# Kernel tuning notes

Measured on AMD Instinct MI355X. Metric: run time of the kernel, lower is better.

The kernel has to match this reference:

```python
import jax, jax.numpy as jnp
import numpy as np

N_NODES = 100000
N_EDGES = 600000
D_IN = 128
HID = 128
N_LAYERS = 3


def gcn_conv(x, W, b, src, dst, num_nodes):
    """PyG-style GCNConv: D^{-1/2}(A+I)D^{-1/2} X W + b (self-loops added)."""
    h = x @ W  # [N, H]
    # in-degree including self-loop
    deg = jnp.zeros((num_nodes,), dtype=x.dtype).at[dst].add(1.0) + 1.0
    dinv = jax.lax.rsqrt(deg)
    norm = dinv[src] * dinv[dst]  # [E]
    msg = h[src] * norm[:, None]  # [E, H] gather + scale
    out = jax.ops.segment_sum(msg, dst, num_segments=num_nodes)  # scatter-add
    out = out + h * (1.0 / deg)[:, None]  # self-loop term (norm = 1/deg)
    return out + b


def setup_inputs() -> dict:
    key = jax.random.key(0)
    ks = jax.random.split(key, 16)
    x = jax.random.normal(ks[0], (N_NODES, D_IN), dtype=jnp.float32)
    edge_index = jax.random.randint(ks[1], (2, N_EDGES), 0, N_NODES, dtype=jnp.int64)
    timestamp = jax.random.uniform(ks[2], (1,), dtype=jnp.float32)
    # GCN layer weights (glorot-ish scale) and biases
    def glorot(k, fan_in, fan_out):
        s = jnp.sqrt(6.0 / (fan_in + fan_out))
        return jax.random.uniform(k, (fan_in, fan_out), minval=-s, maxval=s, dtype=jnp.float32)
    W_gcn = [glorot(ks[3], D_IN, HID), glorot(ks[4], HID, HID), glorot(ks[5], HID, HID)]
    b_gcn = [jnp.zeros((HID,), jnp.float32) for _ in range(N_LAYERS)]
    # temporal gate MLP: Linear(1,H) -> tanh -> Linear(H,H) -> sigmoid
    Wg1 = glorot(ks[6], 1, HID)
    bg1 = jnp.zeros((HID,), jnp.float32)
    Wg2 = glorot(ks[7], HID, HID)
    bg2 = jnp.zeros((HID,), jnp.float32)
    return {
        "x": x, "edge_index": edge_index, "timestamp": timestamp,
        "W0": W_gcn[0], "b0": b_gcn[0],
        "W1": W_gcn[1], "b1": b_gcn[1],
        "W2": W_gcn[2], "b2": b_gcn[2],
        "Wg1": Wg1, "bg1": bg1, "Wg2": Wg2, "bg2": bg2,
    }


def reference(x, edge_index, timestamp, W0, b0, W1, b1, W2, b2, Wg1, bg1, Wg2, bg2):
    src, dst = edge_index[0], edge_index[1]
    num_nodes = x.shape[0]
    # temporal gate: [1,1] -> [1,H], broadcast over nodes
    t = timestamp.reshape(1, 1)
    gate = jax.nn.sigmoid(jnp.tanh(t @ Wg1 + bg1) @ Wg2 + bg2)  # [1, H]
    for (W, b) in ((W0, b0), (W1, b1), (W2, b2)):
        x = gcn_conv(x, W, b, src, dst, num_nodes)
        x = jax.nn.relu(x)
        x = x * gate  # broadcast gate over nodes
        # dropout: identity in eval mode
    return x
```

## Files before the change

kernel.cpp:

```cpp
#include <hip/hip_runtime.h>
#include <hip/hip_bf16.h>
#include <hip/hip_fp16.h>
#include <math.h>


#define D 128

typedef __attribute__((ext_vector_type(8))) short short8;
typedef __attribute__((ext_vector_type(8))) _Float16 half8;
typedef __attribute__((ext_vector_type(4))) float floatx4;

#define RBITS 8
#define RSZ 256
#define SCAP 4096
#define RCAP 4096

__device__ __forceinline__ unsigned bf16_rne(float x) {
    unsigned u = __float_as_uint(x);
    return (u + 0x7FFFu + ((u >> 16) & 1u)) >> 16;
}

__device__ __forceinline__ void gload_lds16(const void* g, void* l) {
    __builtin_amdgcn_global_load_lds(
        (const __attribute__((address_space(1))) unsigned int*)g,
        (__attribute__((address_space(3))) unsigned int*)l, 16, 0, 0);
}

__device__ __forceinline__ float h2f(unsigned short u) {
    return __half2float(__ushort_as_half(u));
}

__device__ __forceinline__ int cap4(int c) { return (c + 3) & ~3; }

__global__ __launch_bounds__(256) void prep_kernel(
    const float* __restrict__ W0, const float* __restrict__ W1,
    const float* __restrict__ W2, short8* __restrict__ Wf_hi,
    short8* __restrict__ Wf_lo,
    const float* __restrict__ t, const float* __restrict__ Wg1,
    const float* __restrict__ bg1, const float* __restrict__ Wg2,
    const float* __restrict__ bg2, float* __restrict__ gate,
    int* __restrict__ cursor2, int B)
{
    int b = blockIdx.x;
    if (b < 24) {
        int f = b * 256 + threadIdx.x;
        int layer = f >> 11;
        int fi = f & 2047;
        int lane = fi & 63;
        int tt = fi >> 6;
        int kc = tt >> 3, n = tt & 7;
        const float* W = (layer == 0) ? W0 : (layer == 1) ? W1 : W2;
        int krow = kc * 32 + (lane >> 4) * 8;
        int col = n * 16 + (lane & 15);
        short8 hv, lv;
        if (layer == 0) {
            #pragma unroll
            for (int j = 0; j < 8; j++) {
                float x = W[(size_t)(krow + j) * D + col];
                unsigned hb = bf16_rne(x);
                float hf = __uint_as_float(hb << 16);
                unsigned lb = bf16_rne(x - hf);
                hv[j] = (short)hb;
                lv[j] = (short)lb;
            }
        } else {
            #pragma unroll
            for (int j = 0; j < 8; j++) {
                float x = W[(size_t)(krow + j) * D + col];
                __half hh = __float2half(x);
                float hf = __half2float(hh);
                __half ll = __float2half(x - hf);
                hv[j] = (short)__half_as_ushort(hh);
                lv[j] = (short)__half_as_ushort(ll);
            }
        }
        Wf_hi[f] = hv;
        Wf_lo[f] = lv;
        return;
    }
    for (int i = threadIdx.x; i < B; i += 256) cursor2[i] = i * SCAP;
    __shared__ float u[D];
    int j = threadIdx.x;
    if (j < D) {
        float tv = t[0];
        u[j] = tanhf(tv * Wg1[j] + bg1[j]);
    }
    __syncthreads();
    if (j < D) {
        float s = bg2[j];
        #pragma unroll 8
        for (int k = 0; k < D; k++) s += u[k] * Wg2[k * D + j];
        gate[j] = 1.0f / (1.0f + expf(-s));
    }
}

#define P1E 16
__global__ __launch_bounds__(256) void binpass_kernel(
    const int* __restrict__ w, int* __restrict__ cursor2,
    int2* __restrict__ stag, int E, int B)
{
    __shared__ int cnt[512];
    __shared__ int base[512];
    __shared__ int flag;
    int tid = threadIdx.x;
    if (tid == 0) {
        int z = 0;
        for (int k = 0; k < 64; k++) z |= w[2 * k + 1];
        flag = (z == 0) ? 1 : 0;
    }
    for (int i = tid; i < B; i += 256) cnt[i] = 0;
    __syncthreads();
    int i64 = flag;
    int e0 = blockIdx.x * (P1E * 256) + tid;
    int s[P1E], d[P1E], lp[P1E];
    #pragma unroll
    for (int k = 0; k < P1E; k++) {
        int e = e0 + k * 256;
        if (e < E) {
            s[k] = i64 ? w[2 * e] : w[e];
            d[k] = i64 ? w[2 * (E + e)] : w[E + e];
            lp[k] = atomicAdd(&cnt[d[k] >> RBITS], 1);
        }
    }
    __syncthreads();
    for (int i = tid; i < B; i += 256)
        base[i] = cnt[i] ? atomicAdd(&cursor2[i], cnt[i]) : 0;
    __syncthreads();
    #pragma unroll
    for (int k = 0; k < P1E; k++) {
        int e = e0 + k * 256;
        if (e < E) {
            int bin = d[k] >> RBITS;
            int idx = base[bin] + lp[k];
            if (idx < (bin + 1) * SCAP)
                stag[idx] = make_int2(s[k], d[k]);
        }
    }
}

__global__ __launch_bounds__(256) void place1_kernel(
    const int2* __restrict__ stag, const int* __restrict__ cursor2,
    int* __restrict__ obeg, int* __restrict__ oend,
    float* __restrict__ dinv, int N)
{
    __shared__ int cnt[RSZ];
    __shared__ int wsum[4], wpre[4];
    int b = blockIdx.x, tid = threadIdx.x;
    int d0 = b * RSZ;
    int nd = (d0 + RSZ < N) ? RSZ : N - d0;
    cnt[tid] = 0;
    __syncthreads();
    int ecount = cursor2[b] - b * SCAP;
    if (ecount > SCAP) ecount = SCAP;
    const int2* sp = stag + (size_t)b * SCAP;
    for (int i = tid; i < ecount; i += 256)
        atomicAdd(&cnt[sp[i].y - d0], 1);
    __syncthreads();
    int c = (tid < nd) ? cnt[tid] : 0;
    int cap = cap4(c);
    int s = cap;
    int lane = tid & 63, wid = tid >> 6;
    #pragma unroll
    for (int off = 1; off < 64; off <<= 1) {
        int n = __shfl_up(s, off);
        if (lane >= off) s += n;
    }
    if (lane == 63) wsum[wid] = s;
    __syncthreads();
    if (tid == 0) {
        int a = 0;
        #pragma unroll
        for (int k = 0; k < 4; k++) { wpre[k] = a; a += wsum[k]; }
    }
    __syncthreads();
    int pre = wpre[wid] + (s - cap);
    if (tid < nd) {
        int beg = b * RCAP + pre;
        obeg[d0 + tid] = beg;
        oend[d0 + tid] = beg + cap;
        dinv[d0 + tid] = rsqrtf((float)(c + 1));
    }
}

__global__ __launch_bounds__(256) void place2_kernel(
    const int2* __restrict__ stag, const int* __restrict__ cursor2,
    const int* __restrict__ obeg, const int* __restrict__ oend,
    const float* __restrict__ dinv, int2* __restrict__ edges8, int N)
{
    __shared__ int2 buf[RCAP];
    __shared__ int loff[RSZ];
    __shared__ int lcnt[RSZ];
    int b = blockIdx.x, tid = threadIdx.x;
    int d0 = b * RSZ;
    int nd = (d0 + RSZ < N) ? RSZ : N - d0;
    if (tid < nd) {
        loff[tid] = obeg[d0 + tid] - b * RCAP;
        lcnt[tid] = 0;
    }
    __syncthreads();
    int totalcap = oend[d0 + nd - 1] - b * RCAP;
    int ecount = cursor2[b] - b * SCAP;
    if (ecount > SCAP) ecount = SCAP;
    const int2* sp = stag + (size_t)b * SCAP;
    int2* out = edges8 + (size_t)b * RCAP;
    if (totalcap <= RCAP) {
        for (int i = tid; i < totalcap; i += 256) buf[i] = make_int2(0, 0);
        __syncthreads();
        for (int i = tid; i < ecount; i += 256) {
            int2 sd = sp[i];
            int ld = sd.y - d0;
            int pos = loff[ld] + atomicAdd(&lcnt[ld], 1);
            buf[pos] = make_int2(sd.x, __float_as_int(dinv[sd.x]));
        }
        __syncthreads();
        for (int i = tid; i < totalcap; i += 256) out[i] = buf[i];
    } else {
        for (int i = tid; i < totalcap && i < RCAP; i += 256)
            out[i] = make_int2(0, 0);
        __syncthreads();
        for (int i = tid; i < ecount; i += 256) {
            int2 sd = sp[i];
            int ld = sd.y - d0;
            int pos = loff[ld] + atomicAdd(&lcnt[ld], 1);
            if (pos < RCAP)
                out[pos] = make_int2(sd.x, __float_as_int(dinv[sd.x]));
        }
    }
}

#define WSTAGE(kc_)                                                           \
    {                                                                         \
        short* wb_ = Wfs + (((kc_) & 1) ? 8192 : 0);                          \
        const short8* gh_ = Wf_hi + (size_t)(kc_) * 512;                      \
        const short8* gl_ = Wf_lo + (size_t)(kc_) * 512;                      \
        _Pragma("unroll")                                                     \
        for (int i_ = 0; i_ < 2; i_++) {                                      \
            int c_ = i_ * 256 + w * 64;                                       \
            gload_lds16(gh_ + c_ + lane, wb_ + c_ * 8);                       \
            gload_lds16(gl_ + c_ + lane, wb_ + 4096 + c_ * 8);                \
        }                                                                     \
    }

#define MFMA_BLOCK(kc)                                                        \
    {                                                                         \
        const short* wb = Wfs + (((kc) & 1) ? 8192 : 0);                      \
        _Pragma("unroll")                                                     \
        for (int n = 0; n < 8; n++) {                                         \
            short8 bh = *(const short8*)(wb + (n * 64 + lane) * 8);           \
            short8 bl = *(const short8*)(wb + 4096 + (n * 64 + lane) * 8);    \
            acc[0][n] = __builtin_amdgcn_mfma_f32_16x16x32_bf16(ah0, bh, acc[0][n], 0, 0, 0); \
            acc[0][n] = __builtin_amdgcn_mfma_f32_16x16x32_bf16(ah0, bl, acc[0][n], 0, 0, 0); \
            acc[0][n] = __builtin_amdgcn_mfma_f32_16x16x32_bf16(al0, bh, acc[0][n], 0, 0, 0); \
            acc[1][n] = __builtin_amdgcn_mfma_f32_16x16x32_bf16(ah1, bh, acc[1][n], 0, 0, 0); \
            acc[1][n] = __builtin_amdgcn_mfma_f32_16x16x32_bf16(ah1, bl, acc[1][n], 0, 0, 0); \
            acc[1][n] = __builtin_amdgcn_mfma_f32_16x16x32_bf16(al1, bh, acc[1][n], 0, 0, 0); \
        }                                                                     \
    }

#define MFMA_BLOCK_F16(kc)                                                    \
    {                                                                         \
        const short* wb = Wfs + (((kc) & 1) ? 8192 : 0);                      \
        _Pragma("unroll")                                                     \
        for (int n = 0; n < 8; n++) {                                         \
            half8 bh = *(const half8*)(wb + (n * 64 + lane) * 8);             \
            half8 bl = *(const half8*)(wb + 4096 + (n * 64 + lane) * 8);      \
            acc[0][n] = __builtin_amdgcn_mfma_f32_16x16x32_f16(ah0, bh, acc[0][n], 0, 0, 0); \
            acc[0][n] = __builtin_amdgcn_mfma_f32_16x16x32_f16(ah0, bl, acc[0][n], 0, 0, 0); \
            acc[1][n] = __builtin_amdgcn_mfma_f32_16x16x32_f16(ah1, bh, acc[1][n], 0, 0, 0); \
            acc[1][n] = __builtin_amdgcn_mfma_f32_16x16x32_f16(ah1, bl, acc[1][n], 0, 0, 0); \
        }                                                                     \
    }

#define EPILOGUE()                                                            \
    _Pragma("unroll")                                                         \
    for (int rt = 0; rt < 2; rt++) {                                          \
        _Pragma("unroll")                                                     \
        for (int reg = 0; reg < 4; reg++) {                                   \
            int row = rowbase + rt * 16 + qd * 4 + reg;                       \
            if (row < M) {                                                    \
                unsigned short* hp = H16 + (size_t)row * D + m16;             \
                _Pragma("unroll")                                             \
                for (int n = 0; n < 8; n++)                                   \
                    hp[n * 16] = __half_as_ushort(__float2half(acc[rt][n][reg])); \
            }                                                                 \
        }                                                                     \
    }

#define GBM 128
__device__ __forceinline__ void cvt8(const float* f, short8& hi, short8& lo) {
    #pragma unroll
    for (int j = 0; j < 8; j++) {
        unsigned hb = bf16_rne(f[j]);
        float hf = __uint_as_float(hb << 16);
        unsigned lb = bf16_rne(f[j] - hf);
        hi[j] = (short)hb;
        lo[j] = (short)lb;
    }
}

__global__ __launch_bounds__(256) void gemm_f32_kernel(
    const float* __restrict__ X, const short8* __restrict__ Wf_hi,
    const short8* __restrict__ Wf_lo, unsigned short* __restrict__ H16, int M)
{
    __shared__ short Wfs[16384];
    int tid = threadIdx.x;
    int w = tid >> 6, lane = tid & 63;
    int m16 = lane & 15, qd = lane >> 4;
    int rowbase = blockIdx.x * GBM + w * 32;

    int r0 = rowbase + m16;      if (r0 >= M) r0 = M - 1;
    int r1 = rowbase + m16 + 16; if (r1 >= M) r1 = M - 1;
    const float* xp0 = X + (size_t)r0 * D + qd * 8;
    const float* xp1 = X + (size_t)r1 * D + qd * 8;

    floatx4 acc[2][8];
    #pragma unroll
    for (int rt = 0; rt < 2; rt++)
        #pragma unroll
        for (int n = 0; n < 8; n++)
            acc[rt][n] = (floatx4)(0.f);

    #define LOADA(kc_, A0, A1)                                              \
        {                                                                   \
            *(float4*)(A0)     = *(const float4*)(xp0 + (kc_) * 32);        \
            *(float4*)(A0 + 4) = *(const float4*)(xp0 + (kc_) * 32 + 4);    \
            *(float4*)(A1)     = *(const float4*)(xp1 + (kc_) * 32);        \
            *(float4*)(A1 + 4) = *(const float4*)(xp1 + (kc_) * 32 + 4);    \
        }

    float a0c[8], a1c[8], a0n[8], a1n[8];
    WSTAGE(0)
    LOADA(0, a0c, a1c)

    #pragma unroll
    for (int kc = 0; kc < 4; kc++) {
        __syncthreads();
        if (kc < 3) {
            WSTAGE(kc + 1)
            LOADA(kc + 1, a0n, a1n)
        }
        short8 ah0, al0, ah1, al1;
        cvt8(a0c, ah0, al0);
        cvt8(a1c, ah1, al1);
        MFMA_BLOCK(kc)
        if (kc < 3) {
            #pragma unroll
            for (int z = 0; z < 8; z++) { a0c[z] = a0n[z]; a1c[z] = a1n[z]; }
        }
    }
    #undef LOADA
    EPILOGUE()
}

__global__ __launch_bounds__(256) void gemm_f16_kernel(
    const unsigned short* __restrict__ Xh,
    const short8* __restrict__ Wf_hi, const short8* __restrict__ Wf_lo,
    unsigned short* __restrict__ H16, int M)
{
    __shared__ short Wfs[16384];
    int tid = threadIdx.x;
    int w = tid >> 6, lane = tid & 63;
    int m16 = lane & 15, qd = lane >> 4;
    int rowbase = blockIdx.x * GBM + w * 32;

    int r0 = rowbase + m16;      if (r0 >= M) r0 = M - 1;
    int r1 = rowbase + m16 + 16; if (r1 >= M) r1 = M - 1;
    const unsigned short* xh0 = Xh + (size_t)r0 * D + qd * 8;
    const unsigned short* xh1 = Xh + (size_t)r1 * D + qd * 8;

    floatx4 acc[2][8];
    #pragma unroll
    for (int rt = 0; rt < 2; rt++)
        #pragma unroll
        for (int n = 0; n < 8; n++)
            acc[rt][n] = (floatx4)(0.f);

    half8 ah0, ah1, nh0, nh1;
    WSTAGE(0)
    ah0 = *(const half8*)(xh0);
    ah1 = *(const half8*)(xh1);

    #pragma unroll
    for (int kc = 0; kc < 4; kc++) {
        __syncthreads();
        if (kc < 3) {
            WSTAGE(kc + 1)
            nh0 = *(const half8*)(xh0 + (kc + 1) * 32);
            nh1 = *(const half8*)(xh1 + (kc + 1) * 32);
        }
        MFMA_BLOCK_F16(kc)
        if (kc < 3) { ah0 = nh0; ah1 = nh1; }
    }
    EPILOGUE()
}

__global__ __launch_bounds__(256) void agg_kernel(
    const unsigned short* __restrict__ H16, const int2* __restrict__ edges,
    const int* __restrict__ obeg, const int* __restrict__ oend,
    const float* __restrict__ dinv,
    const float* __restrict__ bias, const float* __restrict__ gate,
    float* __restrict__ outF, unsigned short* __restrict__ outH,
    int M, int writeF32)
{
    int t = threadIdx.x;
    int hw = t >> 5;
    int l32 = t & 31;
    int node = blockIdx.x * 8 + hw;
    if (node >= M) return;

    int beg = obeg[node];
    int end = oend[node];
    float dv = dinv[node];
    const unsigned short* __restrict__ Hc = H16 + l32 * 4;
    ushort4 us = *(const ushort4*)(Hc + (size_t)node * D);
    float4 acc = make_float4(0.f, 0.f, 0.f, 0.f);

    if (beg < end) {
        int4 p0 = *(const int4*)(edges + beg);
        int4 p1 = *(const int4*)(edges + beg + 2);
        ushort4 u0 = *(const ushort4*)(Hc + (size_t)p0.x * D);
        ushort4 u1 = *(const ushort4*)(Hc + (size_t)p0.z * D);
        ushort4 u2 = *(const ushort4*)(Hc + (size_t)p1.x * D);
        ushort4 u3 = *(const ushort4*)(Hc + (size_t)p1.z * D);
        int j1 = (beg + 4 < end) ? beg + 4 : beg;
        int4 q0 = *(const int4*)(edges + j1);
        int4 q1 = *(const int4*)(edges + j1 + 2);

        for (int j = beg; j < end; j += 4) {
            int jn = j + 8;
            int jp = (jn < end) ? jn : beg;
            int4 r0 = *(const int4*)(edges + jp);
            int4 r1 = *(const int4*)(edges + jp + 2);
            ushort4 v0 = *(const ushort4*)(Hc + (size_t)q0.x * D);
            ushort4 v1 = *(const ushort4*)(Hc + (size_t)q0.z * D);
            ushort4 v2 = *(const ushort4*)(Hc + (size_t)q1.x * D);
            ushort4 v3 = *(const ushort4*)(Hc + (size_t)q1.z * D);
            float n0 = __int_as_float(p0.y) * dv, n1 = __int_as_float(p0.w) * dv;
            float n2 = __int_as_float(p1.y) * dv, n3 = __int_as_float(p1.w) * dv;
            acc.x = fmaf(h2f(u3.x), n3, fmaf(h2f(u2.x), n2, fmaf(h2f(u1.x), n1, fmaf(h2f(u0.x), n0, acc.x))));
            acc.y = fmaf(h2f(u3.y), n3, fmaf(h2f(u2.y), n2, fmaf(h2f(u1.y), n1, fmaf(h2f(u0.y), n0, acc.y))));
            acc.z = fmaf(h2f(u3.z), n3, fmaf(h2f(u2.z), n2, fmaf(h2f(u1.z), n1, fmaf(h2f(u0.z), n0, acc.z))));
            acc.w = fmaf(h2f(u3.w), n3, fmaf(h2f(u2.w), n2, fmaf(h2f(u1.w), n1, fmaf(h2f(u0.w), n0, acc.w))));
            p0 = q0; p1 = q1; q0 = r0; q1 = r1;
            u0 = v0; u1 = v1; u2 = v2; u3 = v3;
        }
    }

    float nself = dv * dv;
    acc.x = fmaf(h2f(us.x), nself, acc.x);
    acc.y = fmaf(h2f(us.y), nself, acc.y);
    acc.z = fmaf(h2f(us.z), nself, acc.z);
    acc.w = fmaf(h2f(us.w), nself, acc.w);

    float4 bv = *(const float4*)(bias + l32 * 4);
    float4 gv = *(const float4*)(gate + l32 * 4);
    acc.x = fmaxf(acc.x + bv.x, 0.f) * gv.x;
    acc.y = fmaxf(acc.y + bv.y, 0.f) * gv.y;
    acc.z = fmaxf(acc.z + bv.z, 0.f) * gv.z;
    acc.w = fmaxf(acc.w + bv.w, 0.f) * gv.w;

    if (writeF32) {
        *(float4*)(outF + (size_t)node * D + l32 * 4) = acc;
    } else {
        ushort4 hs = make_ushort4(
            __half_as_ushort(__float2half(acc.x)),
            __half_as_ushort(__float2half(acc.y)),
            __half_as_ushort(__float2half(acc.z)),
            __half_as_ushort(__float2half(acc.w)));
        *(ushort4*)(outH + (size_t)node * D + l32 * 4) = hs;
    }
}

static inline size_t align_up(size_t v, size_t a) { return (v + a - 1) & ~(a - 1); }

extern "C" void kernel_launch(void* const* d_in, const int* in_sizes, int n_in,
                              void* d_out, int out_size, void* d_ws, size_t ws_size,
                              hipStream_t stream)
{
    const float* x   = (const float*)d_in[0];
    const int*   ei  = (const int*)d_in[1];
    const float* ts  = (const float*)d_in[2];
    const float* Wl[3] = { (const float*)d_in[3], (const float*)d_in[5], (const float*)d_in[7] };
    const float* bl[3] = { (const float*)d_in[4], (const float*)d_in[6], (const float*)d_in[8] };
    const float* Wg1 = (const float*)d_in[9];
    const float* bg1 = (const float*)d_in[10];
    const float* Wg2 = (const float*)d_in[11];
    const float* bg2 = (const float*)d_in[12];

    const int N = in_sizes[0] / D;
    const int E = in_sizes[1] / 2;
    const int B = (N + RSZ - 1) / RSZ;

    char* p = (char*)d_ws;
    unsigned short* h16 = (unsigned short*)p; p += align_up((size_t)N * D * 2, 256);
    unsigned short* xh  = (unsigned short*)p; p += align_up((size_t)N * D * 2, 256);
    float* dinv = (float*)p; p += align_up((size_t)N * 4, 256);
    int* obeg   = (int*)p;   p += align_up((size_t)N * 4, 256);
    int* oend   = (int*)p;   p += align_up((size_t)N * 4, 256);
    int* cursor2 = (int*)p;  p += align_up((size_t)B * 4, 256);
    int2* stag  = (int2*)p;  p += align_up((size_t)B * SCAP * 8, 256);
    int2* edges8 = (int2*)p; p += align_up((size_t)B * RCAP * 8, 256);
    float* gate = (float*)p; p += align_up((size_t)D * 4, 256);
    short8* Wf_hi = (short8*)p; p += align_up((size_t)3 * 2048 * 16, 256);
    short8* Wf_lo = (short8*)p; p += align_up((size_t)3 * 2048 * 16, 256);
    (void)ws_size; (void)n_in; (void)out_size;

    prep_kernel<<<25, 256, 0, stream>>>(
        Wl[0], Wl[1], Wl[2], Wf_hi, Wf_lo,
        ts, Wg1, bg1, Wg2, bg2, gate, cursor2, B);
    int g1 = (E + P1E * 256 - 1) / (P1E * 256);
    binpass_kernel<<<g1, 256, 0, stream>>>(ei, cursor2, stag, E, B);
    place1_kernel<<<B, 256, 0, stream>>>(stag, cursor2, obeg, oend, dinv, N);
    place2_kernel<<<B, 256, 0, stream>>>(stag, cursor2, obeg, oend, dinv, edges8, N);

    int ggrid = (N + GBM - 1) / GBM;
    int agrid = (N + 7) / 8;
    gemm_f32_kernel<<<ggrid, 256, 0, stream>>>(x, Wf_hi, Wf_lo, h16, N);
    agg_kernel<<<agrid, 256, 0, stream>>>(h16, edges8, obeg, oend, dinv, bl[0], gate,
                                          nullptr, xh, N, 0);
    gemm_f16_kernel<<<ggrid, 256, 0, stream>>>(xh, Wf_hi + 2048, Wf_lo + 2048, h16, N);
    agg_kernel<<<agrid, 256, 0, stream>>>(h16, edges8, obeg, oend, dinv, bl[1], gate,
                                          nullptr, xh, N, 0);
    gemm_f16_kernel<<<ggrid, 256, 0, stream>>>(xh, Wf_hi + 4096, Wf_lo + 4096, h16, N);
    agg_kernel<<<agrid, 256, 0, stream>>>(h16, edges8, obeg, oend, dinv, bl[2], gate,
                                          (float*)d_out, nullptr, N, 1);
}
```

Baseline: 197.1 us.

## Fuse neighbor aggregation with next layer's GEMM via shared-memory tile

Layers 1 and 2 now use one kernel per layer instead of two. Each block aggregates 128 nodes, applies bias, ReLU and gate, and stores the fp16 result in a padded LDS tile. It then runs the next layer's MFMA GEMM directly from that tile. This removes the global write and re-read of the intermediate activation and two launches, at the cost of less parallelism in the gather phase (grid of N/128 blocks with 16 serial node iterations), larger LDS use, and an unpipelined weight load per k-chunk.

```diff
diff --git a/kernel.cpp b/kernel.cpp
--- a/kernel.cpp
+++ b/kernel.cpp
@@ -14,6 +14,8 @@
 #define RSZ 256
 #define SCAP 4096
 #define RCAP 4096
+#define GBM 128
+#define APITCH 136
 
 __device__ __forceinline__ unsigned bf16_rne(float x) {
     unsigned u = __float_as_uint(x);
@@ -31,6 +33,49 @@
 }
 
 __device__ __forceinline__ int cap4(int c) { return (c + 3) & ~3; }
+
+__device__ __forceinline__ float4 agg_core(
+    const unsigned short* __restrict__ Hc, const int2* __restrict__ edges,
+    int beg, int end, float dv, int node)
+{
+    ushort4 us = *(const ushort4*)(Hc + (size_t)node * D);
+    float4 acc = make_float4(0.f, 0.f, 0.f, 0.f);
+    if (beg < end) {
+        int4 p0 = *(const int4*)(edges + beg);
+        int4 p1 = *(const int4*)(edges + beg + 2);
+        ushort4 u0 = *(const ushort4*)(Hc + (size_t)p0.x * D);
+        ushort4 u1 = *(const ushort4*)(Hc + (size_t)p0.z * D);
+        ushort4 u2 = *(const ushort4*)(Hc + (size_t)p1.x * D);
+        ushort4 u3 = *(const ushort4*)(Hc + (size_t)p1.z * D);
+        int j1 = (beg + 4 < end) ? beg + 4 : beg;
+        int4 q0 = *(const int4*)(edges + j1);
+        int4 q1 = *(const int4*)(edges + j1 + 2);
+        for (int j = beg; j < end; j += 4) {
+            int jn = j + 8;
+            int jp = (jn < end) ? jn : beg;
+            int4 r0 = *(const int4*)(edges + jp);
+            int4 r1 = *(const int4*)(edges + jp + 2);
+            ushort4 v0 = *(const ushort4*)(Hc + (size_t)q0.x * D);
+            ushort4 v1 = *(const ushort4*)(Hc + (size_t)q0.z * D);
+            ushort4 v2 = *(const ushort4*)(Hc + (size_t)q1.x * D);
+            ushort4 v3 = *(const ushort4*)(Hc + (size_t)q1.z * D);
+            float n0 = __int_as_float(p0.y) * dv, n1 = __int_as_float(p0.w) * dv;
+            float n2 = __int_as_float(p1.y) * dv, n3 = __int_as_float(p1.w) * dv;
+            acc.x = fmaf(h2f(u3.x), n3, fmaf(h2f(u2.x), n2, fmaf(h2f(u1.x), n1, fmaf(h2f(u0.x), n0, acc.x))));
+            acc.y = fmaf(h2f(u3.y), n3, fmaf(h2f(u2.y), n2, fmaf(h2f(u1.y), n1, fmaf(h2f(u0.y), n0, acc.y))));
+            acc.z = fmaf(h2f(u3.z), n3, fmaf(h2f(u2.z), n2, fmaf(h2f(u1.z), n1, fmaf(h2f(u0.z), n0, acc.z))));
+            acc.w = fmaf(h2f(u3.w), n3, fmaf(h2f(u2.w), n2, fmaf(h2f(u1.w), n1, fmaf(h2f(u0.w), n0, acc.w))));
+            p0 = q0; p1 = q1; q0 = r0; q1 = r1;
+            u0 = v0; u1 = v1; u2 = v2; u3 = v3;
+        }
+    }
+    float nself = dv * dv;
+    acc.x = fmaf(h2f(us.x), nself, acc.x);
+    acc.y = fmaf(h2f(us.y), nself, acc.y);
+    acc.z = fmaf(h2f(us.z), nself, acc.z);
+    acc.w = fmaf(h2f(us.w), nself, acc.w);
+    return acc;
+}
 
 __global__ __launch_bounds__(256) void prep_kernel(
     const float* __restrict__ W0, const float* __restrict__ W1,
@@ -241,6 +286,18 @@
         }                                                                     \
     }
 
+#define WSTAGE1(kc_)                                                          \
+    {                                                                         \
+        const short8* gh_ = Wf_hi + (size_t)(kc_) * 512;                      \
+        const short8* gl_ = Wf_lo + (size_t)(kc_) * 512;                      \
+        _Pragma("unroll")                                                     \
+        for (int i_ = 0; i_ < 2; i_++) {                                      \
+            int c_ = i_ * 256 + w * 64;                                       \
+            gload_lds16(gh_ + c_ + lane, Wfs + c_ * 8);                       \
+            gload_lds16(gl_ + c_ + lane, Wfs + 4096 + c_ * 8);                \
+        }                                                                     \
+    }
+
 #define MFMA_BLOCK(kc)                                                        \
     {                                                                         \
         const short* wb = Wfs + (((kc) & 1) ? 8192 : 0);                      \
@@ -257,13 +314,12 @@
         }                                                                     \
     }
 
-#define MFMA_BLOCK_F16(kc)                                                    \
+#define MFMA_BLOCK_F16S()                                                     \
     {                                                                         \
-        const short* wb = Wfs + (((kc) & 1) ? 8192 : 0);                      \
         _Pragma("unroll")                                                     \
         for (int n = 0; n < 8; n++) {                                         \
-            half8 bh = *(const half8*)(wb + (n * 64 + lane) * 8);             \
-            half8 bl = *(const half8*)(wb + 4096 + (n * 64 + lane) * 8);      \
+            half8 bh = *(const half8*)(Wfs + (n * 64 + lane) * 8);            \
+            half8 bl = *(const half8*)(Wfs + 4096 + (n * 64 + lane) * 8);     \
             acc[0][n] = __builtin_amdgcn_mfma_f32_16x16x32_f16(ah0, bh, acc[0][n], 0, 0, 0); \
             acc[0][n] = __builtin_amdgcn_mfma_f32_16x16x32_f16(ah0, bl, acc[0][n], 0, 0, 0); \
             acc[1][n] = __builtin_amdgcn_mfma_f32_16x16x32_f16(ah1, bh, acc[1][n], 0, 0, 0); \
@@ -271,22 +327,6 @@
         }                                                                     \
     }
 
-#define EPILOGUE()                                                            \
-    _Pragma("unroll")                                                         \
-    for (int rt = 0; rt < 2; rt++) {                                          \
-        _Pragma("unroll")                                                     \
-        for (int reg = 0; reg < 4; reg++) {                                   \
-            int row = rowbase + rt * 16 + qd * 4 + reg;                       \
-            if (row < M) {                                                    \
-                unsigned short* hp = H16 + (size_t)row * D + m16;             \
-                _Pragma("unroll")                                             \
-                for (int n = 0; n < 8; n++)                                   \
-                    hp[n * 16] = __half_as_ushort(__float2half(acc[rt][n][reg])); \
-            }                                                                 \
-        }                                                                     \
-    }
-
-#define GBM 128
 __device__ __forceinline__ void cvt8(const float* f, short8& hi, short8& lo) {
     #pragma unroll
     for (int j = 0; j < 8; j++) {
@@ -349,49 +389,99 @@
         }
     }
     #undef LOADA
-    EPILOGUE()
-}
-
-__global__ __launch_bounds__(256) void gemm_f16_kernel(
-    const unsigned short* __restrict__ Xh,
+    #pragma unroll
+    for (int rt = 0; rt < 2; rt++) {
+        #pragma unroll
+        for (int reg = 0; reg < 4; reg++) {
+            int row = rowbase + rt * 16 + qd * 4 + reg;
+            if (row < M) {
+                unsigned short* hp = H16 + (size_t)row * D + m16;
+                #pragma unroll
+                for (int n = 0; n < 8; n++)
+                    hp[n * 16] = __half_as_ushort(__float2half(acc[rt][n][reg]));
+            }
+        }
+    }
+}
+
+__global__ __launch_bounds__(256) void agg_gemm_kernel(
+    const unsigned short* __restrict__ Hin, const int2* __restrict__ edges,
+    const int* __restrict__ obeg, const int* __restrict__ oend,
+    const float* __restrict__ dinv, const float* __restrict__ bias,
+    const float* __restrict__ gate,
     const short8* __restrict__ Wf_hi, const short8* __restrict__ Wf_lo,
-    unsigned short* __restrict__ H16, int M)
-{
-    __shared__ short Wfs[16384];
+    unsigned short* __restrict__ Hout, int M)
+{
+    __shared__ short As[GBM * APITCH];
+    __shared__ short Wfs[8192];
     int tid = threadIdx.x;
-    int w = tid >> 6, lane = tid & 63;
-    int m16 = lane & 15, qd = lane >> 4;
-    int rowbase = blockIdx.x * GBM + w * 32;
-
-    int r0 = rowbase + m16;      if (r0 >= M) r0 = M - 1;
-    int r1 = rowbase + m16 + 16; if (r1 >= M) r1 = M - 1;
-    const unsigned short* xh0 = Xh + (size_t)r0 * D + qd * 8;
-    const unsigned short* xh1 = Xh + (size_t)r1 * D + qd * 8;
-
-    floatx4 acc[2][8];
-    #pragma unroll
-    for (int rt = 0; rt < 2; rt++)
+    int blockrow = blockIdx.x * GBM;
+
+    {
+        int hw = tid >> 5, l32 = tid & 31;
+        const unsigned short* __restrict__ Hc = Hin + l32 * 4;
+        float4 bv = *(const float4*)(bias + l32 * 4);
+        float4 gv = *(const float4*)(gate + l32 * 4);
+        for (int sub = 0; sub < 16; sub++) {
+            int ln = sub * 8 + hw;
+            int node = blockrow + ln;
+            ushort4 hs = make_ushort4(0, 0, 0, 0);
+            if (node < M) {
+                int beg = obeg[node], end = oend[node];
+                float dv = dinv[node];
+                float4 acc = agg_core(Hc, edges, beg, end, dv, node);
+                acc.x = fmaxf(acc.x + bv.x, 0.f) * gv.x;
+                acc.y = fmaxf(acc.y + bv.y, 0.f) * gv.y;
+                acc.z = fmaxf(acc.z + bv.z, 0.f) * gv.z;
+                acc.w = fmaxf(acc.w + bv.w, 0.f) * gv.w;
+                hs = make_ushort4(
+                    __half_as_ushort(__float2half(acc.x)),
+                    __half_as_ushort(__float2half(acc.y)),
+                    __half_as_ushort(__float2half(acc.z)),
+                    __half_as_ushort(__float2half(acc.w)));
+            }
+            *(ushort4*)(As + (size_t)ln * APITCH + l32 * 4) = hs;
+        }
+    }
+    __syncthreads();
+
+    {
+        int w = tid >> 6, lane = tid & 63;
+        int m16 = lane & 15, qd = lane >> 4;
+        int lr0 = w * 32 + m16, lr1 = lr0 + 16;
+        int rowbase = blockrow + w * 32;
+
+        floatx4 acc[2][8];
         #pragma unroll
-        for (int n = 0; n < 8; n++)
-            acc[rt][n] = (floatx4)(0.f);
-
-    half8 ah0, ah1, nh0, nh1;
-    WSTAGE(0)
-    ah0 = *(const half8*)(xh0);
-    ah1 = *(const half8*)(xh1);
-
-    #pragma unroll
-    for (int kc = 0; kc < 4; kc++) {
-        __syncthreads();
-        if (kc < 3) {
-            WSTAGE(kc + 1)
-            nh0 = *(const half8*)(xh0 + (kc + 1) * 32);
-            nh1 = *(const half8*)(xh1 + (kc + 1) * 32);
-        }
-        MFMA_BLOCK_F16(kc)
-        if (kc < 3) { ah0 = nh0; ah1 = nh1; }
-    }
-    EPILOGUE()
+        for (int rt = 0; rt < 2; rt++)
+            #pragma unroll
+            for (int n = 0; n < 8; n++)
+                acc[rt][n] = (floatx4)(0.f);
+
+        #pragma unroll
+        for (int kc = 0; kc < 4; kc++) {
+            WSTAGE1(kc)
+            __syncthreads();
+            half8 ah0 = *(const half8*)(As + (size_t)lr0 * APITCH + kc * 32 + qd * 8);
+            half8 ah1 = *(const half8*)(As + (size_t)lr1 * APITCH + kc * 32 + qd * 8);
+            MFMA_BLOCK_F16S()
+            __syncthreads();
+        }
+
+        #pragma unroll
+        for (int rt = 0; rt < 2; rt++) {
+            #pragma unroll
+            for (int reg = 0; reg < 4; reg++) {
+                int row = rowbase + rt * 16 + qd * 4 + reg;
+                if (row < M) {
+                    unsigned short* hp = Hout + (size_t)row * D + m16;
+                    #pragma unroll
+                    for (int n = 0; n < 8; n++)
+                        hp[n * 16] = __half_as_ushort(__float2half(acc[rt][n][reg]));
+                }
+            }
+        }
+    }
 }
 
 __global__ __launch_bounds__(256) void agg_kernel(
@@ -399,8 +489,7 @@
     const int* __restrict__ obeg, const int* __restrict__ oend,
     const float* __restrict__ dinv,
     const float* __restrict__ bias, const float* __restrict__ gate,
-    float* __restrict__ outF, unsigned short* __restrict__ outH,
-    int M, int writeF32)
+    float* __restrict__ outF, int M)
 {
     int t = threadIdx.x;
     int hw = t >> 5;
@@ -412,45 +501,7 @@
     int end = oend[node];
     float dv = dinv[node];
     const unsigned short* __restrict__ Hc = H16 + l32 * 4;
-    ushort4 us = *(const ushort4*)(Hc + (size_t)node * D);
-    float4 acc = make_float4(0.f, 0.f, 0.f, 0.f);
-
-    if (beg < end) {
-        int4 p0 = *(const int4*)(edges + beg);
-        int4 p1 = *(const int4*)(edges + beg + 2);
-        ushort4 u0 = *(const ushort4*)(Hc + (size_t)p0.x * D);
-        ushort4 u1 = *(const ushort4*)(Hc + (size_t)p0.z * D);
-        ushort4 u2 = *(const ushort4*)(Hc + (size_t)p1.x * D);
-        ushort4 u3 = *(const ushort4*)(Hc + (size_t)p1.z * D);
-        int j1 = (beg + 4 < end) ? beg + 4 : beg;
-        int4 q0 = *(const int4*)(edges + j1);
-        int4 q1 = *(const int4*)(edges + j1 + 2);
-
-        for (int j = beg; j < end; j += 4) {
-            int jn = j + 8;
-            int jp = (jn < end) ? jn : beg;
-            int4 r0 = *(const int4*)(edges + jp);
-            int4 r1 = *(const int4*)(edges + jp + 2);
-            ushort4 v0 = *(const ushort4*)(Hc + (size_t)q0.x * D);
-            ushort4 v1 = *(const ushort4*)(Hc + (size_t)q0.z * D);
-            ushort4 v2 = *(const ushort4*)(Hc + (size_t)q1.x * D);
-            ushort4 v3 = *(const ushort4*)(Hc + (size_t)q1.z * D);
-            float n0 = __int_as_float(p0.y) * dv, n1 = __int_as_float(p0.w) * dv;
-            float n2 = __int_as_float(p1.y) * dv, n3 = __int_as_float(p1.w) * dv;
-            acc.x = fmaf(h2f(u3.x), n3, fmaf(h2f(u2.x), n2, fmaf(h2f(u1.x), n1, fmaf(h2f(u0.x), n0, acc.x))));
-            acc.y = fmaf(h2f(u3.y), n3, fmaf(h2f(u2.y), n2, fmaf(h2f(u1.y), n1, fmaf(h2f(u0.y), n0, acc.y))));
-            acc.z = fmaf(h2f(u3.z), n3, fmaf(h2f(u2.z), n2, fmaf(h2f(u1.z), n1, fmaf(h2f(u0.z), n0, acc.z))));
-            acc.w = fmaf(h2f(u3.w), n3, fmaf(h2f(u2.w), n2, fmaf(h2f(u1.w), n1, fmaf(h2f(u0.w), n0, acc.w))));
-            p0 = q0; p1 = q1; q0 = r0; q1 = r1;
-            u0 = v0; u1 = v1; u2 = v2; u3 = v3;
-        }
-    }
-
-    float nself = dv * dv;
-    acc.x = fmaf(h2f(us.x), nself, acc.x);
-    acc.y = fmaf(h2f(us.y), nself, acc.y);
-    acc.z = fmaf(h2f(us.z), nself, acc.z);
-    acc.w = fmaf(h2f(us.w), nself, acc.w);
+    float4 acc = agg_core(Hc, edges, beg, end, dv, node);
 
     float4 bv = *(const float4*)(bias + l32 * 4);
     float4 gv = *(const float4*)(gate + l32 * 4);
@@ -459,16 +510,7 @@
     acc.z = fmaxf(acc.z + bv.z, 0.f) * gv.z;
     acc.w = fmaxf(acc.w + bv.w, 0.f) * gv.w;
 
-    if (writeF32) {
-        *(float4*)(outF + (size_t)node * D + l32 * 4) = acc;
-    } else {
-        ushort4 hs = make_ushort4(
-            __half_as_ushort(__float2half(acc.x)),
-            __half_as_ushort(__float2half(acc.y)),
-            __half_as_ushort(__float2half(acc.z)),
-            __half_as_ushort(__float2half(acc.w)));
-        *(ushort4*)(outH + (size_t)node * D + l32 * 4) = hs;
-    }
+    *(float4*)(outF + (size_t)node * D + l32 * 4) = acc;
 }
 
 static inline size_t align_up(size_t v, size_t a) { return (v + a - 1) & ~(a - 1); }
@@ -492,8 +534,8 @@
     const int B = (N + RSZ - 1) / RSZ;
 
     char* p = (char*)d_ws;
-    unsigned short* h16 = (unsigned short*)p; p += align_up((size_t)N * D * 2, 256);
-    unsigned short* xh  = (unsigned short*)p; p += align_up((size_t)N * D * 2, 256);
+    unsigned short* h16a = (unsigned short*)p; p += align_up((size_t)N * D * 2, 256);
+    unsigned short* h16b = (unsigned short*)p; p += align_up((size_t)N * D * 2, 256);
     float* dinv = (float*)p; p += align_up((size_t)N * 4, 256);
     int* obeg   = (int*)p;   p += align_up((size_t)N * 4, 256);
     int* oend   = (int*)p;   p += align_up((size_t)N * 4, 256);
@@ -515,13 +557,13 @@
 
     int ggrid = (N + GBM - 1) / GBM;
     int agrid = (N + 7) / 8;
-    gemm_f32_kernel<<<ggrid, 256, 0, stream>>>(x, Wf_hi, Wf_lo, h16, N);
-    agg_kernel<<<agrid, 256, 0, stream>>>(h16, edges8, obeg, oend, dinv, bl[0], gate,
-                                          nullptr, xh, N, 0);
-    gemm_f16_kernel<<<ggrid, 256, 0, stream>>>(xh, Wf_hi + 2048, Wf_lo + 2048, h16, N);
-    agg_kernel<<<agrid, 256, 0, stream>>>(h16, edges8, obeg, oend, dinv, bl[1], gate,
-                                          nullptr, xh, N, 0);
-    gemm_f16_kernel<<<ggrid, 256, 0, stream>>>(xh, Wf_hi + 4096, Wf_lo + 4096, h16, N);
-    agg_kernel<<<agrid, 256, 0, stream>>>(h16, edges8, obeg, oend, dinv, bl[2], gate,
-                                          (float*)d_out, nullptr, N, 1);
-}
+    gemm_f32_kernel<<<ggrid, 256, 0, stream>>>(x, Wf_hi, Wf_lo, h16a, N);
+    agg_gemm_kernel<<<ggrid, 256, 0, stream>>>(h16a, edges8, obeg, oend, dinv,
+                                               bl[0], gate, Wf_hi + 2048, Wf_lo + 2048,
+                                               h16b, N);
+    agg_gemm_kernel<<<ggrid, 256, 0, stream>>>(h16b, edges8, obeg, oend, dinv,
+                                               bl[1], gate, Wf_hi + 4096, Wf_lo + 4096,
+                                               h16a, N);
+    agg_kernel<<<agrid, 256, 0, stream>>>(h16a, edges8, obeg, oend, dinv,
+                                          bl[2], gate, (float*)d_out, N);
+}
```

After: 230.4 us. 16.9% more time.
